# Kernel optimization log

Measured on AMD Instinct MI355X. Metric: run time of the kernel, lower is better.

The kernel has to match this reference:

```python
import math
import jax, jax.numpy as jnp
import numpy as np

MUL = 64
N_ROWS = 131072
L = (0, 1, 2)
# all parity-even triangle-allowed paths (i_in1, i_in2, i_out), connection_mode 'uvu'
PATHS = ((0, 0, 0), (0, 1, 1), (0, 2, 2),
         (1, 0, 1), (1, 1, 0), (1, 1, 1), (1, 1, 2), (1, 2, 1), (1, 2, 2),
         (2, 0, 2), (2, 1, 1), (2, 1, 2), (2, 2, 0), (2, 2, 1), (2, 2, 2))


def _su2_cg(j1, j2, j3, m1, m2, m3):
    # standard SU(2) Clebsch-Gordan coefficient (integer l), matches e3nn
    if m3 != m1 + m2:
        return 0.0
    f = math.factorial
    vmin = max(-j1 + j2 + m3, -j1 + m1, 0)
    vmax = min(j2 + j3 + m1, j3 - j1 + j2, j3 + m3)
    C = math.sqrt((2 * j3 + 1) * f(j3 + j1 - j2) * f(j3 - j1 + j2) * f(j1 + j2 - j3)
                  * f(j3 + m3) * f(j3 - m3)
                  / (f(j1 + j2 + j3 + 1) * f(j1 - m1) * f(j1 + m1) * f(j2 - m2) * f(j2 + m2)))
    S = 0.0
    for v in range(vmin, vmax + 1):
        S += (-1.0) ** (v + j2 + m2) * f(j2 + j3 + m1 - v) * f(j1 - m1 + v) \
             / (f(v) * f(j3 - j1 + j2 - v) * f(j3 + m3 - v) * f(v + j1 - j2 - m3))
    return C * S


def _q(l):
    # change of basis real -> complex spherical harmonics (e3nn convention)
    q = np.zeros((2 * l + 1, 2 * l + 1), dtype=np.complex128)
    for m in range(-l, 0):
        q[l + m, l + abs(m)] = 1 / math.sqrt(2)
        q[l + m, l - abs(m)] = -1j / math.sqrt(2)
    q[l, l] = 1.0
    for m in range(1, l + 1):
        q[l + m, l + abs(m)] = (-1) ** m / math.sqrt(2)
        q[l + m, l - abs(m)] = 1j * (-1) ** m / math.sqrt(2)
    return (-1j) ** l * q


def wigner_3j(l1, l2, l3):
    # real Wigner-3j tensor, Frobenius norm 1, identical to e3nn o3.wigner_3j
    C = np.zeros((2 * l1 + 1, 2 * l2 + 1, 2 * l3 + 1))
    for m1 in range(-l1, l1 + 1):
        for m2 in range(-l2, l2 + 1):
            for m3 in range(-l3, l3 + 1):
                C[l1 + m1, l2 + m2, l3 + m3] = _su2_cg(l1, l2, l3, m1, m2, m3)
    C = C / math.sqrt(2 * l3 + 1)
    W = np.einsum('ij,kl,mn,ikn->jlm', _q(l1), _q(l2), np.conj(_q(l3).T), C.astype(np.complex128))
    assert np.abs(W.imag).max() < 1e-9
    return np.ascontiguousarray(W.real)


# per-path CG tensor with the 'component' normalization coeff sqrt(2*l_out+1) folded in
_W3J = [np.sqrt(2 * L[i3] + 1) * wigner_3j(L[i1], L[i2], L[i3]) for (i1, i2, i3) in PATHS]
# rescale sqrt_k per path: fan_in('uvu') = mul_in2 = 1, summed over paths per out slice
_FAN_IN = {0: 3, 1: 6, 2: 6}
_SQRT_K = np.array([1.0 / math.sqrt(_FAN_IN[i3]) for (_, _, i3) in PATHS], dtype=np.float32)


def setup_inputs() -> dict:
    key = jax.random.key(0)
    k1, k2, k3, k4 = jax.random.split(key, 4)
    x = jax.random.normal(k1, (N_ROWS, 9 * MUL), dtype=jnp.float32)   # 64x0e+64x1e+64x2e
    y = jax.random.normal(k2, (N_ROWS, 9), dtype=jnp.float32)         # 1x0e+1x1e+1x2e
    # internal weights: randn, then scaled in-place by sqrt_k at init (rescale=True)
    weight = jax.random.normal(k3, (len(PATHS), MUL), dtype=jnp.float32) * jnp.asarray(_SQRT_K)[:, None]
    bias = jax.random.normal(k4, (MUL,), dtype=jnp.float32) * 0.02     # bias on the 0e slice
    return {"x": x, "y": y, "weight": weight, "bias": bias}


def reference(x, y, weight, bias):
    N = x.shape[0]
    # split inputs into per-l blocks: [N, mul, 2l+1]
    xs = [x[:, :MUL].reshape(N, MUL, 1),
          x[:, MUL:4 * MUL].reshape(N, MUL, 3),
          x[:, 4 * MUL:9 * MUL].reshape(N, MUL, 5)]
    ys = [y[:, 0:1], y[:, 1:4], y[:, 4:9]]
    outs = [jnp.zeros((N, MUL, d), x.dtype) for d in (1, 3, 5)]
    for p, (i1, i2, i3) in enumerate(PATHS):
        C = jnp.asarray(_W3J[p], dtype=x.dtype)  # [2l1+1, 2l2+1, 2l3+1]
        # 'uvu' path with mul_in2 = 1: out[n,u,k] += w[u] * C[i,j,k] * x[n,u,i] * y[n,j]
        contrib = jnp.einsum('ijk,nui,nj->nuk', C, xs[i1], ys[i2])
        outs[i3] = outs[i3] + contrib * weight[p][None, :, None]
    outs[0] = outs[0] + bias[None, :, None]  # bias only on scalar-even slice
    return jnp.concatenate([o.reshape(N, -1) for o in outs], axis=1)
```

## Files before the change

kernel.cpp:

```cpp
#include <hip/hip_runtime.h>
#include <utility>

namespace w3j {

constexpr int NP = 15;
constexpr int P1[NP] = {0,0,0,1,1,1,1,1,1,2,2,2,2,2,2};
constexpr int P2[NP] = {0,1,2,0,1,1,1,2,2,0,1,1,2,2,2};
constexpr int P3[NP] = {0,1,2,1,0,1,2,1,2,2,1,2,0,1,2};
constexpr int BASE[3] = {0,1,4};

constexpr double cfact(int n){ double r = 1.0; for (int i = 2; i <= n; ++i) r *= i; return r; }
constexpr double csqrt(double x){
  double g = x > 1.0 ? x : 1.0;
  for (int i = 0; i < 64; ++i){ double ng = 0.5*(g + x/g); if (ng == g) break; g = ng; }
  return g;
}
constexpr double neg1pow(int n){ return (n & 1) ? -1.0 : 1.0; }
constexpr int imax3(int a,int b,int c){ int m = a > b ? a : b; return m > c ? m : c; }
constexpr int imin3(int a,int b,int c){ int m = a < b ? a : b; return m < c ? m : c; }

constexpr double su2_cg(int j1,int j2,int j3,int m1,int m2,int m3){
  if (m3 != m1 + m2) return 0.0;
  int vmin = imax3(-j1 + j2 + m3, -j1 + m1, 0);
  int vmax = imin3(j2 + j3 + m1, j3 - j1 + j2, j3 + m3);
  double C = csqrt((2*j3 + 1) * cfact(j3 + j1 - j2) * cfact(j3 - j1 + j2) * cfact(j1 + j2 - j3)
                   * cfact(j3 + m3) * cfact(j3 - m3)
                   / (cfact(j1 + j2 + j3 + 1) * cfact(j1 - m1) * cfact(j1 + m1)
                      * cfact(j2 - m2) * cfact(j2 + m2)));
  double S = 0.0;
  for (int v = vmin; v <= vmax; ++v)
    S += neg1pow(v + j2 + m2) * cfact(j2 + j3 + m1 - v) * cfact(j1 - m1 + v)
         / (cfact(v) * cfact(j3 - j1 + j2 - v) * cfact(j3 + m3 - v) * cfact(v + j1 - j2 - m3));
  return C * S;
}

struct cplx { double re, im; };
constexpr cplx cmul(cplx a, cplx b){ return { a.re*b.re - a.im*b.im, a.re*b.im + a.im*b.re }; }
constexpr cplx cadd(cplx a, cplx b){ return { a.re + b.re, a.im + b.im }; }

struct QM { cplx q[5][5]; };
constexpr QM qmat(int l){
  QM Q{};
  const double is2 = 1.0 / csqrt(2.0);
  for (int m = -l; m < 0; ++m){
    Q.q[l+m][l-m] = cplx{ is2, 0.0 };
    Q.q[l+m][l+m] = cplx{ 0.0, -is2 };
  }
  Q.q[l][l] = cplx{ 1.0, 0.0 };
  for (int m = 1; m <= l; ++m){
    double s = neg1pow(m);
    Q.q[l+m][l+m] = cplx{ s*is2, 0.0 };
    Q.q[l+m][l-m] = cplx{ 0.0, s*is2 };
  }
  cplx f{1.0, 0.0};
  for (int t = 0; t < l; ++t) f = cmul(f, cplx{0.0, -1.0});
  for (int a = 0; a < 2*l+1; ++a) for (int b = 0; b < 2*l+1; ++b) Q.q[a][b] = cmul(Q.q[a][b], f);
  return Q;
}

struct W3 { double w[5][5][5]; };
constexpr W3 wig(int l1,int l2,int l3){
  const int d1 = 2*l1+1, d2 = 2*l2+1, d3 = 2*l3+1;
  double C[5][5][5] = {};
  for (int a = 0; a < d1; ++a) for (int b = 0; b < d2; ++b) for (int c = 0; c < d3; ++c)
    C[a][b][c] = su2_cg(l1, l2, l3, a - l1, b - l2, c - l3);
  const QM q1 = qmat(l1), q2 = qmat(l2), q3 = qmat(l3);
  cplx T1[5][5][5] = {};
  for (int j = 0; j < d1; ++j) for (int k = 0; k < d2; ++k) for (int n = 0; n < d3; ++n){
    cplx s{0,0};
    for (int i = 0; i < d1; ++i) s = cadd(s, cmul(q1.q[i][j], cplx{ C[i][k][n], 0.0 }));
    T1[j][k][n] = s;
  }
  cplx T2[5][5][5] = {};
  for (int j = 0; j < d1; ++j) for (int l = 0; l < d2; ++l) for (int n = 0; n < d3; ++n){
    cplx s{0,0};
    for (int k = 0; k < d2; ++k) s = cadd(s, cmul(q2.q[k][l], T1[j][k][n]));
    T2[j][l][n] = s;
  }
  W3 W{};
  for (int j = 0; j < d1; ++j) for (int l = 0; l < d2; ++l) for (int m = 0; m < d3; ++m){
    cplx s{0,0};
    for (int n = 0; n < d3; ++n)
      s = cadd(s, cmul(cplx{ q3.q[n][m].re, -q3.q[n][m].im }, T2[j][l][n]));
    W.w[j][l][m] = s.re;
  }
  return W;
}

constexpr W3 W_00 = wig(0,0,0);
constexpr W3 W_01 = wig(0,1,1);
constexpr W3 W_02 = wig(0,2,2);
constexpr W3 W_03 = wig(1,0,1);
constexpr W3 W_04 = wig(1,1,0);
constexpr W3 W_05 = wig(1,1,1);
constexpr W3 W_06 = wig(1,1,2);
constexpr W3 W_07 = wig(1,2,1);
constexpr W3 W_08 = wig(1,2,2);
constexpr W3 W_09 = wig(2,0,2);
constexpr W3 W_10 = wig(2,1,1);
constexpr W3 W_11 = wig(2,1,2);
constexpr W3 W_12 = wig(2,2,0);
constexpr W3 W_13 = wig(2,2,1);
constexpr W3 W_14 = wig(2,2,2);

struct Entry { int p, gi, gj, gk; float v; };
struct Table { Entry e[615]; int n; };
constexpr Table build(){
  const W3 WS[NP] = { W_00,W_01,W_02,W_03,W_04,W_05,W_06,W_07,
                      W_08,W_09,W_10,W_11,W_12,W_13,W_14 };
  Table t{};
  for (int p = 0; p < NP; ++p){
    const int l1 = P1[p], l2 = P2[p], l3 = P3[p];
    for (int i = 0; i < 2*l1+1; ++i)
      for (int j = 0; j < 2*l2+1; ++j)
        for (int k = 0; k < 2*l3+1; ++k){
          double v = WS[p].w[i][j][k];
          if (v > 1e-12 || v < -1e-12){
            t.e[t.n] = Entry{ p, BASE[l1] + i, BASE[l2] + j, BASE[l3] + k, (float)v };
            ++t.n;
          }
        }
  }
  return t;
}
constexpr Table TBL = build();
constexpr int NNZ = TBL.n;

}

template<int E>
__device__ __forceinline__ void apply_one(const float (&xx)[9], const float (&yv)[9],
                                          const float (&wp)[w3j::NP], float (&oo)[9]){
  constexpr w3j::Entry en = w3j::TBL.e[E];
  oo[en.gk] = fmaf(wp[en.p] * xx[en.gi] * en.v, yv[en.gj], oo[en.gk]);
}

template<int... Es>
__device__ __forceinline__ void apply_all(std::integer_sequence<int, Es...>,
                                          const float (&xx)[9], const float (&yv)[9],
                                          const float (&wp)[w3j::NP], float (&oo)[9]){
  (apply_one<Es>(xx, yv, wp, oo), ...);
}

constexpr int ROWS = 16;
constexpr int RF   = 576;
constexpr int LDSF = ROWS * RF;
constexpr int V4   = LDSF / 4 / 256;

__global__ __launch_bounds__(256)
void tp_rescale_kernel(const float* __restrict__ x, const float* __restrict__ y,
                       const float* __restrict__ w, const float* __restrict__ b,
                       float* __restrict__ out)
{
  __shared__ float lds[LDSF];
  __shared__ float yl[ROWS * 9];

  const int t = threadIdx.x;
  const long rowbase = (long)blockIdx.x * ROWS;

  {
    const float4* __restrict__ src = (const float4*)(x + rowbase * RF);
    float4* dst = (float4*)lds;
    #pragma unroll
    for (int i = 0; i < V4; ++i) dst[i * 256 + t] = src[i * 256 + t];
    if (t < ROWS * 9) yl[t] = y[rowbase * 9 + t];
  }
  __syncthreads();

  const int u = t & 63;
  const int wv = t >> 6;
  float wp[w3j::NP];
  #pragma unroll
  for (int p = 0; p < w3j::NP; ++p) wp[p] = w[p * 64 + u];
  const float bu = b[u];

  float acc[4][9];
  #pragma unroll
  for (int r = 0; r < 4; ++r) {
    const int lr = wv + 4 * r;
    const float* __restrict__ xr = lds + lr * RF;
    const float* __restrict__ yr = yl + lr * 9;

    float xx[9], yv[9], oo[9];
    xx[0] = xr[u];
    #pragma unroll
    for (int i = 0; i < 3; ++i) xx[1 + i] = xr[64 + 3 * u + i];
    #pragma unroll
    for (int k = 0; k < 5; ++k) xx[4 + k] = xr[256 + 5 * u + k];
    #pragma unroll
    for (int j = 0; j < 9; ++j) yv[j] = yr[j];
    #pragma unroll
    for (int k = 0; k < 9; ++k) oo[k] = 0.0f;

    apply_all(std::make_integer_sequence<int, w3j::NNZ>{}, xx, yv, wp, oo);

    acc[r][0] = oo[0] + bu;
    #pragma unroll
    for (int k = 1; k < 9; ++k) acc[r][k] = oo[k];
  }
  __syncthreads();

  #pragma unroll
  for (int r = 0; r < 4; ++r) {
    const int lr = wv + 4 * r;
    float* __restrict__ orow = lds + lr * RF;
    orow[u] = acc[r][0];
    #pragma unroll
    for (int i = 0; i < 3; ++i) orow[64 + 3 * u + i] = acc[r][1 + i];
    #pragma unroll
    for (int k = 0; k < 5; ++k) orow[256 + 5 * u + k] = acc[r][4 + k];
  }
  __syncthreads();

  {
    float4* __restrict__ dst = (float4*)(out + rowbase * RF);
    const float4* src = (const float4*)lds;
    #pragma unroll
    for (int i = 0; i < V4; ++i) dst[i * 256 + t] = src[i * 256 + t];
  }
}

extern "C" void kernel_launch(void* const* d_in, const int* in_sizes, int n_in,
                              void* d_out, int out_size, void* d_ws, size_t ws_size,
                              hipStream_t stream) {
  const float* x = (const float*)d_in[0];
  const float* y = (const float*)d_in[1];
  const float* w = (const float*)d_in[2];
  const float* b = (const float*)d_in[3];
  float* out = (float*)d_out;

  const int nrows = in_sizes[0] / 576;
  const int blocks = nrows / ROWS;

  hipLaunchKernelGGL(tp_rescale_kernel, dim3(blocks), dim3(256), 0, stream,
                     x, y, w, b, out);
}
```

Before: 127.0 us.

## Make each wavefront own its rows in LDS and drop block barriers

Each 64-lane wavefront now loads, computes and stores its own 4 contiguous rows in a private LDS slice, so all three __syncthreads are replaced by compiler memory fences. The y values are read straight from global memory instead of being staged in LDS, and results are written back in place over the x rows without holding them in an accumulator array. This removes block-wide barrier stalls and lets waves in a block run independently, which gives better overlap of memory and compute. The risk is that it relies on wave-local LDS ordering within a wavefront, and the per-row y loads from global are scalar-uniform, which may add latency.

After: 118.6 us. 1.07x faster.

```diff
diff --git a/kernel.cpp b/kernel.cpp
--- a/kernel.cpp
+++ b/kernel.cpp
@@ -142,44 +142,44 @@
   (apply_one<Es>(xx, yv, wp, oo), ...);
 }
 
-constexpr int ROWS = 16;
-constexpr int RF   = 576;
-constexpr int LDSF = ROWS * RF;
-constexpr int V4   = LDSF / 4 / 256;
+constexpr int WROWS = 4;
+constexpr int ROWS  = 16;
+constexpr int RF    = 576;
+constexpr int WF    = WROWS * RF;
+constexpr int WV4   = WF / 4 / 64;
 
 __global__ __launch_bounds__(256)
 void tp_rescale_kernel(const float* __restrict__ x, const float* __restrict__ y,
                        const float* __restrict__ w, const float* __restrict__ b,
                        float* __restrict__ out)
 {
-  __shared__ float lds[LDSF];
-  __shared__ float yl[ROWS * 9];
-
-  const int t = threadIdx.x;
-  const long rowbase = (long)blockIdx.x * ROWS;
+  __shared__ float lds[ROWS * RF];
+
+  const int t    = threadIdx.x;
+  const int lane = t & 63;
+  const int wv   = __builtin_amdgcn_readfirstlane(t >> 6);
+  const long rowbase = (long)blockIdx.x * ROWS + wv * WROWS;
+
+  float* wlds = lds + wv * WF;
 
   {
     const float4* __restrict__ src = (const float4*)(x + rowbase * RF);
-    float4* dst = (float4*)lds;
-    #pragma unroll
-    for (int i = 0; i < V4; ++i) dst[i * 256 + t] = src[i * 256 + t];
-    if (t < ROWS * 9) yl[t] = y[rowbase * 9 + t];
-  }
-  __syncthreads();
-
-  const int u = t & 63;
-  const int wv = t >> 6;
+    float4* dst = (float4*)wlds;
+    #pragma unroll
+    for (int i = 0; i < WV4; ++i) dst[i * 64 + lane] = src[i * 64 + lane];
+  }
+  asm volatile("" ::: "memory");
+
+  const int u = lane;
   float wp[w3j::NP];
   #pragma unroll
   for (int p = 0; p < w3j::NP; ++p) wp[p] = w[p * 64 + u];
   const float bu = b[u];
 
-  float acc[4][9];
   #pragma unroll
-  for (int r = 0; r < 4; ++r) {
-    const int lr = wv + 4 * r;
-    const float* __restrict__ xr = lds + lr * RF;
-    const float* __restrict__ yr = yl + lr * 9;
+  for (int r = 0; r < WROWS; ++r) {
+    float* xr = wlds + r * RF;
+    const float* yr = y + (rowbase + r) * 9;
 
     float xx[9], yv[9], oo[9];
     xx[0] = xr[u];
@@ -194,29 +194,19 @@
 
     apply_all(std::make_integer_sequence<int, w3j::NNZ>{}, xx, yv, wp, oo);
 
-    acc[r][0] = oo[0] + bu;
-    #pragma unroll
-    for (int k = 1; k < 9; ++k) acc[r][k] = oo[k];
-  }
-  __syncthreads();
-
-  #pragma unroll
-  for (int r = 0; r < 4; ++r) {
-    const int lr = wv + 4 * r;
-    float* __restrict__ orow = lds + lr * RF;
-    orow[u] = acc[r][0];
-    #pragma unroll
-    for (int i = 0; i < 3; ++i) orow[64 + 3 * u + i] = acc[r][1 + i];
-    #pragma unroll
-    for (int k = 0; k < 5; ++k) orow[256 + 5 * u + k] = acc[r][4 + k];
-  }
-  __syncthreads();
+    xr[u] = oo[0] + bu;
+    #pragma unroll
+    for (int i = 0; i < 3; ++i) xr[64 + 3 * u + i] = oo[1 + i];
+    #pragma unroll
+    for (int k = 0; k < 5; ++k) xr[256 + 5 * u + k] = oo[4 + k];
+  }
+  asm volatile("" ::: "memory");
 
   {
+    const float4* src = (const float4*)wlds;
     float4* __restrict__ dst = (float4*)(out + rowbase * RF);
-    const float4* src = (const float4*)lds;
-    #pragma unroll
-    for (int i = 0; i < V4; ++i) dst[i * 256 + t] = src[i * 256 + t];
+    #pragma unroll
+    for (int i = 0; i < WV4; ++i) dst[i * 64 + lane] = src[i * 64 + lane];
   }
 }
 
```
